# Performance work log

Measured on AMD Instinct MI355X. Metric: run time of the kernel, lower is better.

Reference implementation:

```python
import jax, jax.numpy as jnp
import numpy as np

B, S, H, D = 2, 2048, 16, 64


def setup_inputs() -> dict:
    key = jax.random.key(0)
    ks = jax.random.split(key, 6)
    query = jax.random.normal(ks[0], (B, S, H, D), dtype=jnp.float32)
    k = jax.random.normal(ks[1], (B, S, H, D), dtype=jnp.float32)
    v = jax.random.normal(ks[2], (B, S, H, D), dtype=jnp.float32)
    r = jax.random.normal(ks[3], (B, S, H, D), dtype=jnp.float32)
    r_bias = jax.random.normal(ks[4], (H, D), dtype=jnp.float32)
    r_w_bias = jax.random.normal(ks[5], (H, D), dtype=jnp.float32)
    # causal mask, broadcast over batch and heads; mask==0 positions are filled with -1e9
    mask = jnp.tril(jnp.ones((S, S), dtype=jnp.int32))[None, None, :, :]
    return {"query": query, "key": k, "value": v, "r": r,
            "r_bias": r_bias, "r_w_bias": r_w_bias, "mask": mask}


def reference(query, key, value, r, r_bias, r_w_bias, mask):
    b, s, h, d = query.shape
    # content-based and position-based query terms (Transformer-XL u/v biases)
    rw_head_q = jnp.transpose(query + r_w_bias, (0, 2, 1, 3))  # [B,H,S,D]
    rr_head_q = jnp.transpose(query + r_bias, (0, 2, 1, 3))    # [B,H,S,D]
    k_t = jnp.transpose(key, (0, 2, 1, 3))                     # [B,H,S,D]
    r_t = jnp.transpose(r.reshape(b, -1, h, d), (0, 2, 1, 3))  # [B,H,R,D]
    AC = jnp.einsum('bhqd,bhkd->bhqk', rw_head_q, k_t)
    BD = jnp.einsum('bhqd,bhkd->bhqk', rr_head_q, r_t)
    scores = (AC + BD) * (1.0 / np.sqrt(d).astype(np.float32))
    scores = jnp.where(mask == 0, jnp.float32(-1e9), scores)
    p_attn = jax.nn.softmax(scores, axis=-1)
    v_t = jnp.transpose(value, (0, 2, 1, 3))                   # [B,H,S,D]
    out = jnp.einsum('bhqk,bhkd->bhqd', p_attn, v_t)
    return out, p_attn
```

## Files before the change

kernel.cpp:

```cpp
#include <hip/hip_runtime.h>
#include <hip/hip_fp16.h>

#define S_LEN 2048
#define DHEAD 64
#define NBH   32
#define NHEADS 16

typedef _Float16 half_t;
typedef half_t half8  __attribute__((ext_vector_type(8)));
typedef half_t half4v __attribute__((ext_vector_type(4)));
typedef __fp16 fp16x2 __attribute__((ext_vector_type(2)));
typedef float  f32x16 __attribute__((ext_vector_type(16)));
typedef float  f32x4  __attribute__((ext_vector_type(4)));

#define QSCALE 0.18033688011112042f

__global__ __launch_bounds__(256) void prep_kernel(
    const float* __restrict__ q, const float* __restrict__ k,
    const float* __restrict__ v, const float* __restrict__ r,
    const float* __restrict__ r_bias, const float* __restrict__ r_w_bias,
    half_t* __restrict__ qh, half_t* __restrict__ krh,
    half_t* __restrict__ vt, float* __restrict__ c2)
{
    __shared__ float vtile[64][65];
    int blk = blockIdx.x;
    int st  = blk & 31;
    int bh  = blk >> 5;
    int b = bh >> 4, h = bh & 15;
    int s0 = st * 64;
    int t = threadIdx.x;
    int dg = t & 15;
    int rw = t >> 4;
    const float4 ub = *(const float4*)(r_w_bias + h * 64 + 4 * dg);
    const float4 vb = *(const float4*)(r_bias   + h * 64 + 4 * dg);
    #pragma unroll
    for (int ps = 0; ps < 4; ++ps) {
        int row = ps * 16 + rw;
        size_t iidx = ((size_t)((b * S_LEN + s0 + row) * NHEADS + h)) * DHEAD + 4 * dg;
        float4 qv = *(const float4*)(q + iidx);
        float4 kv = *(const float4*)(k + iidx);
        float4 rv = *(const float4*)(r + iidx);
        float4 vv = *(const float4*)(v + iidx);
        size_t oidx = ((size_t)(bh * S_LEN + s0 + row)) * DHEAD + 4 * dg;
        half4v hq  = { (half_t)(qv.x * QSCALE), (half_t)(qv.y * QSCALE),
                       (half_t)(qv.z * QSCALE), (half_t)(qv.w * QSCALE) };
        half4v hkr = { (half_t)(kv.x + rv.x), (half_t)(kv.y + rv.y),
                       (half_t)(kv.z + rv.z), (half_t)(kv.w + rv.w) };
        *(half4v*)(qh  + oidx) = hq;
        *(half4v*)(krh + oidx) = hkr;
        vtile[4 * dg + 0][row] = vv.x;
        vtile[4 * dg + 1][row] = vv.y;
        vtile[4 * dg + 2][row] = vv.z;
        vtile[4 * dg + 3][row] = vv.w;
        float part = ub.x * kv.x + ub.y * kv.y + ub.z * kv.z + ub.w * kv.w
                   + vb.x * rv.x + vb.y * rv.y + vb.z * rv.z + vb.w * rv.w;
        #pragma unroll
        for (int mm = 1; mm <= 8; mm <<= 1) part += __shfl_xor(part, mm, 64);
        if (dg == 0) c2[(size_t)bh * S_LEN + s0 + row] = part * QSCALE;
    }
    __syncthreads();
    {
        int d = t >> 2, j0 = (t & 3) * 16;
        const float* src = &vtile[d][j0];
        half8 h0, h1;
        #pragma unroll
        for (int e = 0; e < 8; ++e) { h0[e] = (half_t)src[e]; h1[e] = (half_t)src[8 + e]; }
        half_t* dst = vt + ((size_t)(bh * DHEAD + d)) * S_LEN + s0 + j0;
        *(half8*)(dst)     = h0;
        *(half8*)(dst + 8) = h1;
    }
}

__global__ __launch_bounds__(256) void attn_kernel(
    const half_t* __restrict__ qh, const half_t* __restrict__ krh,
    const half_t* __restrict__ vt, const float* __restrict__ c2,
    float* __restrict__ dout)
{
    int wid = threadIdx.x >> 6;
    int bb  = blockIdx.x;
    int swz = (bb & 7) * 64 + (bb >> 3);
    int x4  = swz * 4 + wid;
    int bh  = x4 >> 6;
    int u   = x4 & 63;
    int qt  = (bh & 2) ? (63 - u) : u;
    int i0  = qt * 32;
    int lane = threadIdx.x & 63;
    int lo = lane & 31, hi = lane >> 5;
    int qrow = i0 + lo;

    const half_t* qp = qh  + ((size_t)(bh * S_LEN + i0)) * DHEAD;
    const half_t* kp = krh + ((size_t)bh * S_LEN) * DHEAD;
    const half_t* vp = vt  + ((size_t)bh * DHEAD) * S_LEN;
    const float*  cp = c2  + (size_t)bh * S_LEN;
    float* pout = dout + (size_t)NBH * S_LEN * DHEAD
                       + (size_t)bh * S_LEN * S_LEN
                       + (size_t)qrow * S_LEN + 4 * hi;
    float* oout = dout + ((size_t)(bh * S_LEN + i0)) * DHEAD;

    {
        f32x4 zz = {};
        for (int tt = qt + 1; tt < 64; ++tt) {
            #pragma unroll
            for (int g = 0; g < 4; ++g)
                *(f32x4*)(pout + tt * 32 + 8 * g) = zz;
        }
    }

    half8 qf[4];
    #pragma unroll
    for (int ds = 0; ds < 4; ++ds)
        qf[ds] = *(const half8*)(qp + lo * DHEAD + ds * 16 + hi * 8);

    auto loadK = [&](half8* kf, int t) {
        const half_t* base = kp + (size_t)(t * 32 + lo) * DHEAD + hi * 8;
        #pragma unroll
        for (int ds = 0; ds < 4; ++ds)
            kf[ds] = *(const half8*)(base + ds * 16);
    };
    auto loadV = [&](half8* vv, int t) {
        const half_t* r0 = vp + (size_t)lo * S_LEN + t * 32 + hi * 8;
        const half_t* r1 = vp + (size_t)(lo + 32) * S_LEN + t * 32 + hi * 8;
        vv[0] = *(const half8*)(r0);
        vv[1] = *(const half8*)(r0 + 16);
        vv[2] = *(const half8*)(r1);
        vv[3] = *(const half8*)(r1 + 16);
    };
    auto scoreT = [&](const half8* kf) {
        f32x16 acc = {};
        #pragma unroll
        for (int ds = 0; ds < 4; ++ds)
            acc = __builtin_amdgcn_mfma_f32_32x32x16_f16(kf[ds], qf[ds], acc, 0, 0, 0);
        return acc;
    };

    float Zs = 0.f;
    auto zTile = [&](int t, const half8* kf) {
        f32x16 acc = scoreT(kf);
        int jb = t * 32;
        float zs = 0.f;
        #pragma unroll
        for (int g = 0; g < 4; ++g) {
            f32x4 cv = *(const f32x4*)(cp + jb + 8 * g + 4 * hi);
            #pragma unroll
            for (int e = 0; e < 4; ++e) {
                float ev = exp2f(acc[4 * g + e] + cv[e]);
                if (t == qt) {
                    int j = jb + e + 8 * g + 4 * hi;
                    if (j > qrow) ev = 0.f;
                }
                zs += ev;
            }
        }
        Zs += zs;
    };
    {
        half8 kfA[4], kfB[4];
        loadK(kfA, 0);
        int t = 0;
        while (true) {
            if (t < qt) loadK(kfB, t + 1);
            zTile(t, kfA);
            if (++t > qt) break;
            if (t < qt) loadK(kfA, t + 1);
            zTile(t, kfB);
            if (++t > qt) break;
        }
    }
    float Zrow = Zs + __shfl_xor(Zs, 32, 64);
    float L = log2f(Zrow);

    f32x16 oa0 = {}, oa1 = {};
    auto pvTile = [&](int t, const half8* kf, const half8* vv) {
        f32x16 acc = scoreT(kf);
        int jb = t * 32;
        float p[16];
        #pragma unroll
        for (int g = 0; g < 4; ++g) {
            f32x4 cv = *(const f32x4*)(cp + jb + 8 * g + 4 * hi);
            #pragma unroll
            for (int e = 0; e < 4; ++e)
                p[4 * g + e] = exp2f(acc[4 * g + e] + cv[e] - L);
        }
        if (t == qt) {
            #pragma unroll
            for (int xx = 0; xx < 16; ++xx) {
                int j = jb + (xx & 3) + 8 * (xx >> 2) + 4 * hi;
                if (j > qrow) p[xx] = 0.f;
            }
        }
        #pragma unroll
        for (int g = 0; g < 4; ++g) {
            f32x4 st4 = { p[4 * g], p[4 * g + 1], p[4 * g + 2], p[4 * g + 3] };
            *(f32x4*)(pout + jb + 8 * g) = st4;
        }
        unsigned int wds[8];
        #pragma unroll
        for (int g2 = 0; g2 < 8; ++g2) {
            union { fp16x2 h; unsigned int u; } pk;
            pk.h = __builtin_amdgcn_cvt_pkrtz(p[2 * g2], p[2 * g2 + 1]);
            wds[g2] = pk.u;
        }
        unsigned int pw[8];
        #pragma unroll
        for (int g2 = 0; g2 < 8; ++g2) pw[g2] = __shfl_xor(wds[g2], 32, 64);
        union { unsigned int uu[4]; half8 h; } pa0, pa1;
        pa0.uu[0] = hi ? pw[2]  : wds[0];
        pa0.uu[1] = hi ? pw[3]  : wds[1];
        pa0.uu[2] = hi ? wds[2] : pw[0];
        pa0.uu[3] = hi ? wds[3] : pw[1];
        pa1.uu[0] = hi ? pw[6]  : wds[4];
        pa1.uu[1] = hi ? pw[7]  : wds[5];
        pa1.uu[2] = hi ? wds[6] : pw[4];
        pa1.uu[3] = hi ? wds[7] : pw[5];
        oa0 = __builtin_amdgcn_mfma_f32_32x32x16_f16(pa0.h, vv[0], oa0, 0, 0, 0);
        oa0 = __builtin_amdgcn_mfma_f32_32x32x16_f16(pa1.h, vv[1], oa0, 0, 0, 0);
        oa1 = __builtin_amdgcn_mfma_f32_32x32x16_f16(pa0.h, vv[2], oa1, 0, 0, 0);
        oa1 = __builtin_amdgcn_mfma_f32_32x32x16_f16(pa1.h, vv[3], oa1, 0, 0, 0);
    };
    {
        half8 kfA[4], kfB[4], vA[4], vB[4];
        loadK(kfA, 0); loadV(vA, 0);
        int t = 0;
        while (true) {
            if (t < qt) { loadK(kfB, t + 1); loadV(vB, t + 1); }
            pvTile(t, kfA, vA);
            if (++t > qt) break;
            if (t < qt) { loadK(kfA, t + 1); loadV(vA, t + 1); }
            pvTile(t, kfB, vB);
            if (++t > qt) break;
        }
    }

    #pragma unroll
    for (int xx = 0; xx < 16; ++xx) {
        int row = (xx & 3) + 8 * (xx >> 2) + 4 * hi;
        oout[(size_t)row * DHEAD + lo]      = oa0[xx];
        oout[(size_t)row * DHEAD + 32 + lo] = oa1[xx];
    }
}

extern "C" void kernel_launch(void* const* d_in, const int* in_sizes, int n_in,
                              void* d_out, int out_size, void* d_ws, size_t ws_size,
                              hipStream_t stream)
{
    const float* q   = (const float*)d_in[0];
    const float* k   = (const float*)d_in[1];
    const float* v   = (const float*)d_in[2];
    const float* r   = (const float*)d_in[3];
    const float* rb  = (const float*)d_in[4];
    const float* rwb = (const float*)d_in[5];
    float* out = (float*)d_out;

    char* ws = (char*)d_ws;
    half_t* qh  = (half_t*)(ws);
    half_t* krh = (half_t*)(ws + (size_t) 8 * 1024 * 1024);
    half_t* vtp = (half_t*)(ws + (size_t)16 * 1024 * 1024);
    float*  c2  = (float*) (ws + (size_t)24 * 1024 * 1024);

    hipLaunchKernelGGL(prep_kernel, dim3(1024), dim3(256), 0, stream,
                       q, k, v, r, rb, rwb, qh, krh, vtp, c2);
    hipLaunchKernelGGL(attn_kernel, dim3(512), dim3(256), 0, stream,
                       qh, krh, vtp, c2, out);
}
```

Before: 782.4 us.

## Split each query tile's key loop across four waves with LDS reduction

Each block now handles a single 32-row query tile, and its four waves take interleaved key tiles (stride 4) instead of each wave owning a whole query tile. The softmax denominators and the partial PV accumulators are combined across waves through shared memory, and the grid grows fourfold with heaviest tiles scheduled first. This is meant to shorten the long serial per-wave loop and balance the causal workload. The cost is extra LDS traffic, several block barriers, and idle waves on tiles with few key blocks.

```diff
diff --git a/kernel.cpp b/kernel.cpp
--- a/kernel.cpp
+++ b/kernel.cpp
@@ -76,14 +76,14 @@
     const half_t* __restrict__ vt, const float* __restrict__ c2,
     float* __restrict__ dout)
 {
-    int wid = threadIdx.x >> 6;
+    __shared__ float zl[4][64];
+    __shared__ f32x4 pvred[2][8][64];
+
     int bb  = blockIdx.x;
-    int swz = (bb & 7) * 64 + (bb >> 3);
-    int x4  = swz * 4 + wid;
-    int bh  = x4 >> 6;
-    int u   = x4 & 63;
-    int qt  = (bh & 2) ? (63 - u) : u;
+    int bh  = (bb & 7) * 4 + ((bb >> 3) & 3);
+    int qt  = 63 - (bb >> 5);
     int i0  = qt * 32;
+    int w    = threadIdx.x >> 6;
     int lane = threadIdx.x & 63;
     int lo = lane & 31, hi = lane >> 5;
     int qrow = i0 + lo;
@@ -99,7 +99,7 @@
 
     {
         f32x4 zz = {};
-        for (int tt = qt + 1; tt < 64; ++tt) {
+        for (int tt = qt + 1 + w; tt < 64; tt += 4) {
             #pragma unroll
             for (int g = 0; g < 4; ++g)
                 *(f32x4*)(pout + tt * 32 + 8 * g) = zz;
@@ -155,18 +155,23 @@
     };
     {
         half8 kfA[4], kfB[4];
-        loadK(kfA, 0);
-        int t = 0;
-        while (true) {
-            if (t < qt) loadK(kfB, t + 1);
+        int t = w;
+        if (t <= qt) loadK(kfA, t);
+        while (t <= qt) {
+            if (t + 4 <= qt) loadK(kfB, t + 4);
             zTile(t, kfA);
-            if (++t > qt) break;
-            if (t < qt) loadK(kfA, t + 1);
+            t += 4;
+            if (t > qt) break;
+            if (t + 4 <= qt) loadK(kfA, t + 4);
             zTile(t, kfB);
-            if (++t > qt) break;
-        }
-    }
-    float Zrow = Zs + __shfl_xor(Zs, 32, 64);
+            t += 4;
+        }
+    }
+    zl[w][lane] = Zs;
+    __syncthreads();
+    float Zrow = 0.f;
+    #pragma unroll
+    for (int w2 = 0; w2 < 4; ++w2) Zrow += zl[w2][lo] + zl[w2][lo + 32];
     float L = log2f(Zrow);
 
     f32x16 oa0 = {}, oa1 = {};
@@ -219,23 +224,64 @@
     };
     {
         half8 kfA[4], kfB[4], vA[4], vB[4];
-        loadK(kfA, 0); loadV(vA, 0);
-        int t = 0;
-        while (true) {
-            if (t < qt) { loadK(kfB, t + 1); loadV(vB, t + 1); }
+        int t = w;
+        if (t <= qt) { loadK(kfA, t); loadV(vA, t); }
+        while (t <= qt) {
+            if (t + 4 <= qt) { loadK(kfB, t + 4); loadV(vB, t + 4); }
             pvTile(t, kfA, vA);
-            if (++t > qt) break;
-            if (t < qt) { loadK(kfA, t + 1); loadV(vA, t + 1); }
+            t += 4;
+            if (t > qt) break;
+            if (t + 4 <= qt) { loadK(kfA, t + 4); loadV(vA, t + 4); }
             pvTile(t, kfB, vB);
-            if (++t > qt) break;
-        }
-    }
-
-    #pragma unroll
-    for (int xx = 0; xx < 16; ++xx) {
-        int row = (xx & 3) + 8 * (xx >> 2) + 4 * hi;
-        oout[(size_t)row * DHEAD + lo]      = oa0[xx];
-        oout[(size_t)row * DHEAD + 32 + lo] = oa1[xx];
+            t += 4;
+        }
+    }
+
+    __syncthreads();
+    if (w >= 2) {
+        #pragma unroll
+        for (int j = 0; j < 4; ++j) {
+            f32x4 c0 = { oa0[4*j], oa0[4*j+1], oa0[4*j+2], oa0[4*j+3] };
+            f32x4 c1 = { oa1[4*j], oa1[4*j+1], oa1[4*j+2], oa1[4*j+3] };
+            pvred[w - 2][j][lane]     = c0;
+            pvred[w - 2][j + 4][lane] = c1;
+        }
+    }
+    __syncthreads();
+    if (w < 2) {
+        #pragma unroll
+        for (int j = 0; j < 4; ++j) {
+            f32x4 c0 = pvred[w][j][lane];
+            f32x4 c1 = pvred[w][j + 4][lane];
+            #pragma unroll
+            for (int e = 0; e < 4; ++e) { oa0[4*j+e] += c0[e]; oa1[4*j+e] += c1[e]; }
+        }
+    }
+    __syncthreads();
+    if (w == 1) {
+        #pragma unroll
+        for (int j = 0; j < 4; ++j) {
+            f32x4 c0 = { oa0[4*j], oa0[4*j+1], oa0[4*j+2], oa0[4*j+3] };
+            f32x4 c1 = { oa1[4*j], oa1[4*j+1], oa1[4*j+2], oa1[4*j+3] };
+            pvred[0][j][lane]     = c0;
+            pvred[0][j + 4][lane] = c1;
+        }
+    }
+    __syncthreads();
+    if (w == 0) {
+        #pragma unroll
+        for (int j = 0; j < 4; ++j) {
+            f32x4 c0 = pvred[0][j][lane];
+            f32x4 c1 = pvred[0][j + 4][lane];
+            #pragma unroll
+            for (int e = 0; e < 4; ++e) { oa0[4*j+e] += c0[e]; oa1[4*j+e] += c1[e]; }
+        }
+        #pragma unroll
+        for (int xx = 0; xx < 16; ++xx) {
+            int row = (xx & 3) + 8 * (xx >> 2) + 4 * hi;
+            oout[(size_t)row * DHEAD + lo]      = oa0[xx];
+            oout[(size_t)row * DHEAD + 32 + lo] = oa1[xx];
+        }
     }
 }
 
@@ -259,6 +305,6 @@
 
     hipLaunchKernelGGL(prep_kernel, dim3(1024), dim3(256), 0, stream,
                        q, k, v, r, rb, rwb, qh, krh, vtp, c2);
-    hipLaunchKernelGGL(attn_kernel, dim3(512), dim3(256), 0, stream,
+    hipLaunchKernelGGL(attn_kernel, dim3(2048), dim3(256), 0, stream,
                        qh, krh, vtp, c2, out);
 }
```

After: 706.9 us. 9.6% less time.
